# Kernel optimization log

Hardware: AMD Instinct MI355X
Metric: run time of the kernel (lower is better)

The kernel has to match this reference:

```python
import itertools
import jax, jax.numpy as jnp
import numpy as np

EPS = 1e-15
B, K, H, W = 64, 8, 128, 128


def setup_inputs() -> dict:
    key = jax.random.key(0)
    k1, k2 = jax.random.split(key)
    pred_masks = jax.random.uniform(k1, (B, K, H, W), dtype=jnp.float32)
    aug_masks = jax.random.uniform(k2, (B, K, H, W), dtype=jnp.float32)
    return {"pred_masks": pred_masks, "aug_masks": aug_masks}


def _mask_kl_div(pred, true):
    # true * (log(true+eps) - log(pred+eps)), mean over (H, W)
    return (true * (jnp.log(true + EPS) - jnp.log(pred + EPS))).mean(axis=(-2, -1))


# all K! permutations, precomputed once (K=8 -> 40320 perms)
_PERMS = jnp.asarray(np.array(list(itertools.permutations(range(K))), dtype=np.int32))


def reference(pred_masks, aug_masks):
    b, k, h, w = pred_masks.shape
    t = aug_masks  # targets are detached in torch for the cost matrix
    # Fused pairwise KL cost matrix (avoids the (B,K,K,H,W) broadcast):
    # C[b,i,j] = mean_hw[ t_j*log(t_j+eps) ] - mean_hw[ t_j*log(p_i+eps) ]
    ent = (t * jnp.log(t + EPS)).mean(axis=(-2, -1))          # (B, K) over j
    cross = jnp.einsum('bjhw,bihw->bij', t, jnp.log(pred_masks + EPS)) / (h * w)
    C = ent[:, None, :] - cross                                # (B, K, K)
    # exact linear assignment via exhaustive search over K! permutations
    rows = jnp.arange(k)
    costs = C[:, rows[None, :], _PERMS].sum(axis=-1)           # (B, K!)
    R2C = _PERMS[jnp.argmin(costs, axis=1)]                    # (B, K) col for each row
    # permute rows: out[b, i] = pred[b, argsort(R2C)[b, i]]
    row_perm = jnp.argsort(R2C, axis=1)
    pred_perm = jnp.take_along_axis(pred_masks, row_perm[:, :, None, None], axis=1)
    l = _mask_kl_div(pred_perm, t)                             # (B, K)
    return l.mean(), pred_perm[..., None]
```

## Files before the change

### kernel.cpp

```cpp
#include <hip/hip_runtime.h>


#define BB 64
#define KK 8
#define HW 16384
#define SPANS 8
#define SPAN 2048
#define EPSF 1e-15f

struct MaskTab {
    unsigned char masks[255];
    int off[9];
};

constexpr MaskTab make_tab() {
    MaskTab t{};
    int idx = 0;
    for (int p = 1; p <= 8; ++p) {
        t.off[p - 1] = idx;
        for (int m = 1; m < 256; ++m) {
            int c = 0;
            for (int b = 0; b < 8; ++b) c += (m >> b) & 1;
            if (c == p) t.masks[idx++] = (unsigned char)m;
        }
    }
    t.off[8] = idx;
    return t;
}

__constant__ MaskTab kTab = make_tab();

__device__ __forceinline__ float dot4(float4 t, float4 l) {
    return t.x * l.x + t.y * l.y + t.z * l.z + t.w * l.w;
}

__device__ __forceinline__ float4 log4(float4 a) {
    float4 r;
    r.x = __logf(a.x + EPSF); r.y = __logf(a.y + EPSF);
    r.z = __logf(a.z + EPSF); r.w = __logf(a.w + EPSF);
    return r;
}

__global__ __launch_bounds__(256) void cost_kernel(const float* __restrict__ pred,
                                                   const float* __restrict__ aug,
                                                   float* __restrict__ part,
                                                   float* __restrict__ out)
{
    __shared__ float red[4][72];

    const int blk  = blockIdx.x;
    const int b    = blk >> 3;
    const int s    = blk & 7;
    const int tid  = threadIdx.x;
    const int wave = tid >> 6;
    const int lane = tid & 63;

    if (blk == 0 && tid == 0) out[0] = 0.f;

    const size_t base = (size_t)b * (KK * HW);

    float acc[64];
#pragma unroll
    for (int v = 0; v < 64; ++v) acc[v] = 0.f;
    float ent[8];
#pragma unroll
    for (int j = 0; j < 8; ++j) ent[j] = 0.f;

#pragma unroll
    for (int it = 0; it < 2; ++it) {
        const int e = s * SPAN + (it * 256 + tid) * 4;
        const float* pp = pred + base + e;
        const float* ap = aug  + base + e;

        float4 lp[8];
#pragma unroll
        for (int i = 0; i < 8; ++i)
            lp[i] = log4(*(const float4*)(pp + (size_t)i * HW));

#pragma unroll
        for (int j = 0; j < 8; ++j) {
            const float4 a  = *(const float4*)(ap + (size_t)j * HW);
            ent[j] += dot4(a, log4(a));
#pragma unroll
            for (int i = 0; i < 8; ++i)
                acc[i * 8 + j] += dot4(a, lp[i]);
        }
    }

#pragma unroll
    for (int r = 0; r < 6; ++r) {
        const int d    = 1 << r;
        const int half = 32 >> r;
        const bool hi  = (lane & d) != 0;
#pragma unroll
        for (int k = 0; k < half; ++k) {
            const float send = hi ? acc[k] : acc[k + half];
            const float recv = __shfl_xor(send, d);
            acc[k] = (hi ? acc[k + half] : acc[k]) + recv;
        }
    }

#pragma unroll
    for (int r = 0; r < 3; ++r) {
        const int d    = 1 << r;
        const int half = 4 >> r;
        const bool hi  = (lane & d) != 0;
#pragma unroll
        for (int k = 0; k < half; ++k) {
            const float send = hi ? ent[k] : ent[k + half];
            const float recv = __shfl_xor(send, d);
            ent[k] = (hi ? ent[k + half] : ent[k]) + recv;
        }
    }
    float ev = ent[0];
    ev += __shfl_xor(ev, 8);
    ev += __shfl_xor(ev, 16);
    ev += __shfl_xor(ev, 32);

    const int vidx = ((lane & 1) << 5) | ((lane & 2) << 3) | ((lane & 4) << 1) |
                     ((lane & 8) >> 1) | ((lane & 16) >> 3) | ((lane & 32) >> 5);
    red[wave][vidx] = acc[0];
    if (lane < 8)
        red[wave][64 + (((lane & 1) << 2) | (lane & 2) | ((lane & 4) >> 2))] = ev;
    __syncthreads();

    if (tid < 72) {
        const float ssum = red[0][tid] + red[1][tid] + red[2][tid] + red[3][tid];
        part[(size_t)blk * 72 + tid] = ssum;
    }
}

__global__ __launch_bounds__(256) void permute_kernel(const float* __restrict__ pred,
                                                      const float* __restrict__ part,
                                                      float* __restrict__ out)
{
    __shared__ float red[72];
    __shared__ float C[64];
    __shared__ float dp[256];
    __shared__ int   choice[256];
    __shared__ int   inv8[8];

    const int p    = blockIdx.x;
    const int b    = p >> 3;
    const int tid  = threadIdx.x;

    const float* pb = part + (size_t)b * SPANS * 72;
    if (tid < 72) {
        float s = 0.f;
#pragma unroll
        for (int c = 0; c < SPANS; ++c) s += pb[c * 72 + tid];
        red[tid] = s;
    }
    if (tid == 0) dp[0] = 0.f;
    __syncthreads();
    if (tid < 64) C[tid] = red[64 + (tid & 7)] - red[tid];
    __syncthreads();

    const int grp = tid >> 3;
    const int j   = tid & 7;
    for (int lvl = 1; lvl <= 8; ++lvl) {
        const int start = kTab.off[lvl - 1];
        const int end   = kTab.off[lvl];
        const float* Crow = &C[(lvl - 1) * 8];
        for (int bse = start; bse < end; bse += 32) {
            const int mi = bse + grp;
            if (mi < end) {
                const int M = kTab.masks[mi];
                float v  = 1e30f;
                int   bj = 0;
                if (M & (1 << j)) {
                    v  = dp[M ^ (1 << j)] + Crow[j];
                    bj = j;
                }
#pragma unroll
                for (int d = 1; d < 8; d <<= 1) {
                    const float ov = __shfl_xor(v, d);
                    const int   oj = __shfl_xor(bj, d);
                    if (ov < v) { v = ov; bj = oj; }
                }
                if (j == 0) { dp[M] = v; choice[M] = bj; }
            }
        }
        __syncthreads();
    }

    if (tid == 0) {
        int mask = 255;
        for (int r = 7; r >= 0; --r) {
            const int jj = choice[mask];
            inv8[jj] = r;
            mask ^= 1 << jj;
        }
        if ((p & 7) == 0)
            atomicAdd(out, dp[255] * (1.0f / (16384.0f * 512.0f)));
    }
    __syncthreads();

    const int src_row = inv8[p & 7];
    const float* src  = pred + ((size_t)(b << 3) + src_row) * HW;
    float*      drow  = out + 1 + (size_t)p * HW;

#pragma unroll
    for (int m = 0; m < 16; ++m) {
        const int f = tid + 256 * m;
        const int e = 3 + 4 * f;
        if (f < 4095) {
            float4 v;
            v.x = src[e]; v.y = src[e + 1]; v.z = src[e + 2]; v.w = src[e + 3];
            *(float4*)(drow + e) = v;
        } else {
            drow[0] = src[0]; drow[1] = src[1]; drow[2] = src[2];
            drow[16383] = src[16383];
        }
    }
}

extern "C" void kernel_launch(void* const* d_in, const int* in_sizes, int n_in,
                              void* d_out, int out_size, void* d_ws, size_t ws_size,
                              hipStream_t stream) {
    const float* pred = (const float*)d_in[0];
    const float* aug  = (const float*)d_in[1];
    float* out = (float*)d_out;
    float* part = (float*)d_ws;

    cost_kernel<<<dim3(BB * SPANS), dim3(256), 0, stream>>>(pred, aug, part, out);
    permute_kernel<<<dim3(512), dim3(256), 0, stream>>>(pred, part, out);
}
```

Measured before the change: 118.9 us.

## Double-buffer cost kernel inputs through LDS with async global-to-LDS loads

```diff
diff --git a/kernel.cpp b/kernel.cpp
--- a/kernel.cpp
+++ b/kernel.cpp
@@ -4,8 +4,10 @@
 #define BB 64
 #define KK 8
 #define HW 16384
-#define SPANS 8
-#define SPAN 2048
+#define SPANS 4
+#define SPAN 4096
+#define WIN 1024
+#define NWIN 4
 #define EPSF 1e-15f
 
 struct MaskTab {
@@ -46,18 +48,39 @@
                                                    float* __restrict__ part,
                                                    float* __restrict__ out)
 {
+    __shared__ float tile[2][16][WIN];
     __shared__ float red[4][72];
 
     const int blk  = blockIdx.x;
-    const int b    = blk >> 3;
-    const int s    = blk & 7;
+    const int b    = blk >> 2;
+    const int s    = blk & 3;
     const int tid  = threadIdx.x;
     const int wave = tid >> 6;
     const int lane = tid & 63;
 
     if (blk == 0 && tid == 0) out[0] = 0.f;
 
-    const size_t base = (size_t)b * (KK * HW);
+    const size_t base = (size_t)b * (KK * HW) + (size_t)s * SPAN;
+    const int e4 = lane * 4;
+
+#define STAGE(w)                                                                          \
+    {                                                                                     \
+        const int pb_ = (w) & 1;                                                          \
+        _Pragma("unroll")                                                                 \
+        for (int k = 0; k < 4; ++k) {                                                     \
+            const int vr = 4 * wave + k;                                                  \
+            const float* rp = ((vr < 8) ? (pred + base + (size_t)vr * HW)                 \
+                                        : (aug + base + (size_t)(vr - 8) * HW))           \
+                              + (w) * WIN;                                                \
+            _Pragma("unroll")                                                             \
+            for (int c = 0; c < 4; ++c) {                                                 \
+                __builtin_amdgcn_global_load_lds(                                         \
+                    (const __attribute__((address_space(1))) void*)(rp + c * 256 + e4),   \
+                    (__attribute__((address_space(3))) void*)&tile[pb_][vr][c * 256 + e4],\
+                    16, 0, 0);                                                            \
+            }                                                                             \
+        }                                                                                 \
+    }
 
     float acc[64];
 #pragma unroll
@@ -66,26 +89,31 @@
 #pragma unroll
     for (int j = 0; j < 8; ++j) ent[j] = 0.f;
 
-#pragma unroll
-    for (int it = 0; it < 2; ++it) {
-        const int e = s * SPAN + (it * 256 + tid) * 4;
-        const float* pp = pred + base + e;
-        const float* ap = aug  + base + e;
+    STAGE(0)
+
+#pragma unroll
+    for (int w = 0; w < NWIN; ++w) {
+        __syncthreads();
+        if (w + 1 < NWIN) STAGE(w + 1)
+
+        const int pb = w & 1;
+        const int q4 = tid * 4;
 
         float4 lp[8];
 #pragma unroll
         for (int i = 0; i < 8; ++i)
-            lp[i] = log4(*(const float4*)(pp + (size_t)i * HW));
+            lp[i] = log4(*(const float4*)&tile[pb][i][q4]);
 
 #pragma unroll
         for (int j = 0; j < 8; ++j) {
-            const float4 a  = *(const float4*)(ap + (size_t)j * HW);
+            const float4 a = *(const float4*)&tile[pb][8 + j][q4];
             ent[j] += dot4(a, log4(a));
 #pragma unroll
             for (int i = 0; i < 8; ++i)
                 acc[i * 8 + j] += dot4(a, lp[i]);
         }
     }
+#undef STAGE
 
 #pragma unroll
     for (int r = 0; r < 6; ++r) {
```

After: 129.4 us. 8.8% more time.

## Run permutation DP in last-arriving cost block, leaving copy kernel lightweight

Applied to the files above, without the earlier changes.

```diff
diff --git a/kernel.cpp b/kernel.cpp
--- a/kernel.cpp
+++ b/kernel.cpp
@@ -30,6 +30,8 @@
 
 __constant__ MaskTab kTab = make_tab();
 
+__device__ int g_cnt[64];
+
 __device__ __forceinline__ float dot4(float4 t, float4 l) {
     return t.x * l.x + t.y * l.y + t.z * l.z + t.w * l.w;
 }
@@ -44,18 +46,22 @@
 __global__ __launch_bounds__(256) void cost_kernel(const float* __restrict__ pred,
                                                    const float* __restrict__ aug,
                                                    float* __restrict__ part,
-                                                   float* __restrict__ out)
+                                                   float* __restrict__ loss_part,
+                                                   int*   __restrict__ invtab)
 {
-    __shared__ float red[4][72];
-
-    const int blk  = blockIdx.x;
-    const int b    = blk >> 3;
-    const int s    = blk & 7;
+    __shared__ float red1[4][72];
+    __shared__ int   islast;
+    __shared__ float red[72];
+    __shared__ float C[64];
+    __shared__ float dp[256];
+    __shared__ int   choice[256];
+
+    const int p    = blockIdx.x;
+    const int b    = p >> 3;
+    const int s    = p & 7;
     const int tid  = threadIdx.x;
     const int wave = tid >> 6;
     const int lane = tid & 63;
-
-    if (blk == 0 && tid == 0) out[0] = 0.f;
 
     const size_t base = (size_t)b * (KK * HW);
 
@@ -119,37 +125,32 @@
 
     const int vidx = ((lane & 1) << 5) | ((lane & 2) << 3) | ((lane & 4) << 1) |
                      ((lane & 8) >> 1) | ((lane & 16) >> 3) | ((lane & 32) >> 5);
-    red[wave][vidx] = acc[0];
+    red1[wave][vidx] = acc[0];
     if (lane < 8)
-        red[wave][64 + (((lane & 1) << 2) | (lane & 2) | ((lane & 4) >> 2))] = ev;
+        red1[wave][64 + (((lane & 1) << 2) | (lane & 2) | ((lane & 4) >> 2))] = ev;
     __syncthreads();
 
     if (tid < 72) {
-        const float ssum = red[0][tid] + red[1][tid] + red[2][tid] + red[3][tid];
-        part[(size_t)blk * 72 + tid] = ssum;
-    }
-}
-
-__global__ __launch_bounds__(256) void permute_kernel(const float* __restrict__ pred,
-                                                      const float* __restrict__ part,
-                                                      float* __restrict__ out)
-{
-    __shared__ float red[72];
-    __shared__ float C[64];
-    __shared__ float dp[256];
-    __shared__ int   choice[256];
-    __shared__ int   inv8[8];
-
-    const int p    = blockIdx.x;
-    const int b    = p >> 3;
-    const int tid  = threadIdx.x;
+        const float ssum = red1[0][tid] + red1[1][tid] + red1[2][tid] + red1[3][tid];
+        part[(size_t)p * 72 + tid] = ssum;
+    }
+    __threadfence();
+    __syncthreads();
+
+    if (tid == 0) {
+        const int old = atomicAdd(&g_cnt[b], 1);
+        islast = ((old & 7) == 7);
+    }
+    __syncthreads();
+    if (!islast) return;
+    __threadfence();
 
     const float* pb = part + (size_t)b * SPANS * 72;
     if (tid < 72) {
-        float s = 0.f;
-#pragma unroll
-        for (int c = 0; c < SPANS; ++c) s += pb[c * 72 + tid];
-        red[tid] = s;
+        float sv = 0.f;
+#pragma unroll
+        for (int c = 0; c < SPANS; ++c) sv += pb[c * 72 + tid];
+        red[tid] = sv;
     }
     if (tid == 0) dp[0] = 0.f;
     __syncthreads();
@@ -188,15 +189,30 @@
         int mask = 255;
         for (int r = 7; r >= 0; --r) {
             const int jj = choice[mask];
-            inv8[jj] = r;
+            invtab[b * 8 + jj] = r;
             mask ^= 1 << jj;
         }
-        if ((p & 7) == 0)
-            atomicAdd(out, dp[255] * (1.0f / (16384.0f * 512.0f)));
-    }
-    __syncthreads();
-
-    const int src_row = inv8[p & 7];
+        loss_part[b] = dp[255];
+    }
+}
+
+__global__ __launch_bounds__(256) void copy_kernel(const float* __restrict__ pred,
+                                                   const float* __restrict__ loss_part,
+                                                   const int*   __restrict__ invtab,
+                                                   float* __restrict__ out)
+{
+    const int p   = blockIdx.x;
+    const int b   = p >> 3;
+    const int tid = threadIdx.x;
+
+    if (p == 0 && tid < 64) {
+        float lv = loss_part[tid];
+#pragma unroll
+        for (int d = 1; d < 64; d <<= 1) lv += __shfl_xor(lv, d);
+        if (tid == 0) out[0] = lv * (1.0f / (16384.0f * 512.0f));
+    }
+
+    const int src_row = invtab[p];
     const float* src  = pred + ((size_t)(b << 3) + src_row) * HW;
     float*      drow  = out + 1 + (size_t)p * HW;
 
@@ -220,9 +236,12 @@
                               hipStream_t stream) {
     const float* pred = (const float*)d_in[0];
     const float* aug  = (const float*)d_in[1];
-    float* out = (float*)d_out;
-    float* part = (float*)d_ws;
-
-    cost_kernel<<<dim3(BB * SPANS), dim3(256), 0, stream>>>(pred, aug, part, out);
-    permute_kernel<<<dim3(512), dim3(256), 0, stream>>>(pred, part, out);
-}
+    float* out  = (float*)d_out;
+
+    float* part      = (float*)d_ws;
+    float* loss_part = part + 512 * 72;
+    int*   invtab    = (int*)(loss_part + 64);
+
+    cost_kernel<<<dim3(BB * SPANS), dim3(256), 0, stream>>>(pred, aug, part, loss_part, invtab);
+    copy_kernel<<<dim3(512), dim3(256), 0, stream>>>(pred, loss_part, invtab, out);
+}
```

Result: slower. 163.8 us (+37.8%).
